# Optimization experiments

Hardware: AMD Instinct MI355X
Metric: run time of the kernel (lower is better)

## Reference

```python
import jax, jax.numpy as jnp
import numpy as np

EPS = 1e-06

def setup_inputs() -> dict:
    key = jax.random.key(0)
    k1, k2 = jax.random.split(key)
    x = jax.random.normal(k1, (8192, 4096), dtype=jnp.float32)
    # nn.Linear weight: [num_experts, input_dim]
    W = jax.random.normal(k2, (64, 4096), dtype=jnp.float32) * (1.0 / np.sqrt(4096.0))
    return {"x": x, "W": W}


def reference(x, W):
    # logits: [N, E]  (thin GEMM)
    logits = jnp.einsum('nd,ed->ne', x, W)
    gates = jax.nn.softmax(logits, axis=-1)
    # importance auxiliary loss: per-expert column sums, unbiased std (torch default)
    importance = gates.sum(axis=0)                      # [E]
    mean_imp = importance.mean()
    E = importance.shape[0]
    std_imp = jnp.sqrt(jnp.sum((importance - mean_imp) ** 2) / (E - 1))
    aux_loss = (std_imp / (mean_imp + EPS)) ** 2
    # top-k gates, renormalize with a second softmax
    top_k_gates, top_k_indices = jax.lax.top_k(gates, 2)  # [N, k]
    combine_weights = jax.nn.softmax(top_k_gates, axis=-1)
    return combine_weights, top_k_indices, aux_loss
```

## Files before the change

kernel.cpp:

```cpp
#include <hip/hip_runtime.h>
#include <math.h>

#define NROWS 8192
#define NK    4096
#define NE    64
#define NWV   8

typedef _Float16 f16x8 __attribute__((ext_vector_type(8)));
typedef float    f32x4 __attribute__((ext_vector_type(4)));

__global__ __launch_bounds__(256) void k_prep(const float* __restrict__ W,
                                              _Float16* __restrict__ Whi,
                                              _Float16* __restrict__ Wlo,
                                              float* __restrict__ imp) {
  const int idx = blockIdx.x * 256 + threadIdx.x;
  if (idx < NE) imp[idx] = 0.f;
  const int j    = idx & 7;
  const int lane = (idx >> 3) & 63;
  const int nt   = (idx >> 9) & 3;
  const int ksg  = idx >> 11;
  const int e = nt * 16 + (lane & 15);
  const int k = ksg * 32 + (lane >> 4) * 8 + j;
  const float w = W[(size_t)e * NK + k];
  const _Float16 wh = (_Float16)w;
  const _Float16 wl = (_Float16)(w - (float)wh);
  Whi[idx] = wh;
  Wlo[idx] = wl;
}

__global__ __launch_bounds__(512, 1) void k_fused(const float* __restrict__ x,
                                                  const _Float16* __restrict__ Whi,
                                                  const _Float16* __restrict__ Wlo,
                                                  float* __restrict__ out,
                                                  float* __restrict__ imp) {
  __shared__ float plds[NWV][32][64];
  __shared__ float logit[32][64];
  __shared__ float simp[NWV][64];

  const int tid  = threadIdx.x;
  const int lane = tid & 63;
  const int wv   = __builtin_amdgcn_readfirstlane(tid >> 6);
  const int l15  = lane & 15;
  const int lhi  = lane >> 4;
  const int rbase = blockIdx.x * 32;
  const int k0    = wv * 512;

  const float* __restrict__ xp0 = x + (size_t)(rbase + l15) * NK + k0 + lhi * 8;
  const float* __restrict__ xp1 = xp0 + (size_t)16 * NK;

  f32x4 acc0[4], acc1[4];
#pragma unroll
  for (int nt = 0; nt < 4; ++nt) {
    acc0[nt] = (f32x4){0.f, 0.f, 0.f, 0.f};
    acc1[nt] = (f32x4){0.f, 0.f, 0.f, 0.f};
  }

#pragma unroll 2
  for (int ks = 0; ks < 16; ++ks) {
    const float4 a0 = *(const float4*)(xp0 + ks * 32);
    const float4 a1 = *(const float4*)(xp0 + ks * 32 + 4);
    const float4 b0 = *(const float4*)(xp1 + ks * 32);
    const float4 b1 = *(const float4*)(xp1 + ks * 32 + 4);
    f16x8 ah, al, bh, bl;
    ah[0] = (_Float16)a0.x; al[0] = (_Float16)(a0.x - (float)ah[0]);
    ah[1] = (_Float16)a0.y; al[1] = (_Float16)(a0.y - (float)ah[1]);
    ah[2] = (_Float16)a0.z; al[2] = (_Float16)(a0.z - (float)ah[2]);
    ah[3] = (_Float16)a0.w; al[3] = (_Float16)(a0.w - (float)ah[3]);
    ah[4] = (_Float16)a1.x; al[4] = (_Float16)(a1.x - (float)ah[4]);
    ah[5] = (_Float16)a1.y; al[5] = (_Float16)(a1.y - (float)ah[5]);
    ah[6] = (_Float16)a1.z; al[6] = (_Float16)(a1.z - (float)ah[6]);
    ah[7] = (_Float16)a1.w; al[7] = (_Float16)(a1.w - (float)ah[7]);
    bh[0] = (_Float16)b0.x; bl[0] = (_Float16)(b0.x - (float)bh[0]);
    bh[1] = (_Float16)b0.y; bl[1] = (_Float16)(b0.y - (float)bh[1]);
    bh[2] = (_Float16)b0.z; bl[2] = (_Float16)(b0.z - (float)bh[2]);
    bh[3] = (_Float16)b0.w; bl[3] = (_Float16)(b0.w - (float)bh[3]);
    bh[4] = (_Float16)b1.x; bl[4] = (_Float16)(b1.x - (float)bh[4]);
    bh[5] = (_Float16)b1.y; bl[5] = (_Float16)(b1.y - (float)bh[5]);
    bh[6] = (_Float16)b1.z; bl[6] = (_Float16)(b1.z - (float)bh[6]);
    bh[7] = (_Float16)b1.w; bl[7] = (_Float16)(b1.w - (float)bh[7]);

    const int gk = wv * 16 + ks;
    const size_t boff = ((size_t)(gk * 4) * 64 + lane) * 8;
    f16x8 wh_[4], wl_[4];
#pragma unroll
    for (int nt = 0; nt < 4; ++nt) {
      wh_[nt] = *(const f16x8*)(Whi + boff + nt * 512);
      wl_[nt] = *(const f16x8*)(Wlo + boff + nt * 512);
    }
#pragma unroll
    for (int nt = 0; nt < 4; ++nt) {
      acc0[nt] = __builtin_amdgcn_mfma_f32_16x16x32_f16(ah, wh_[nt], acc0[nt], 0, 0, 0);
      acc1[nt] = __builtin_amdgcn_mfma_f32_16x16x32_f16(bh, wh_[nt], acc1[nt], 0, 0, 0);
    }
#pragma unroll
    for (int nt = 0; nt < 4; ++nt) {
      acc0[nt] = __builtin_amdgcn_mfma_f32_16x16x32_f16(ah, wl_[nt], acc0[nt], 0, 0, 0);
      acc1[nt] = __builtin_amdgcn_mfma_f32_16x16x32_f16(bh, wl_[nt], acc1[nt], 0, 0, 0);
    }
#pragma unroll
    for (int nt = 0; nt < 4; ++nt) {
      acc0[nt] = __builtin_amdgcn_mfma_f32_16x16x32_f16(al, wh_[nt], acc0[nt], 0, 0, 0);
      acc1[nt] = __builtin_amdgcn_mfma_f32_16x16x32_f16(bl, wh_[nt], acc1[nt], 0, 0, 0);
    }
  }

#pragma unroll
  for (int nt = 0; nt < 4; ++nt)
#pragma unroll
    for (int r = 0; r < 4; ++r) {
      plds[wv][lhi * 4 + r][nt * 16 + l15]      = acc0[nt][r];
      plds[wv][16 + lhi * 4 + r][nt * 16 + l15] = acc1[nt][r];
    }
  __syncthreads();

#pragma unroll
  for (int i = 0; i < 4; ++i) {
    const int elem = tid + i * 512;
    const int row  = elem >> 6;
    const int col  = elem & 63;
    const float s01 = plds[0][row][col] + plds[1][row][col];
    const float s23 = plds[2][row][col] + plds[3][row][col];
    const float s45 = plds[4][row][col] + plds[5][row][col];
    const float s67 = plds[6][row][col] + plds[7][row][col];
    logit[row][col] = ((s01 + s23) + (s45 + s67));
  }
  __syncthreads();

  float impacc = 0.f;
#pragma unroll 1
  for (int i = 0; i < 4; ++i) {
    const int rl  = wv * 4 + i;
    const int row = rbase + rl;
    const float lg = logit[rl][lane];

    float m = lg;
#pragma unroll
    for (int d = 1; d < 64; d <<= 1) m = fmaxf(m, __shfl_xor(m, d));
    float p = expf(lg - m);
    float s = p;
#pragma unroll
    for (int d = 1; d < 64; d <<= 1) s += __shfl_xor(s, d);
    const float gate = p / s;
    impacc += gate;

    const unsigned long long key =
        ((unsigned long long)__float_as_uint(gate) << 32) | (unsigned)(63 - lane);
    unsigned long long k1 = key;
#pragma unroll
    for (int d = 1; d < 64; d <<= 1) {
      unsigned long long o = __shfl_xor(k1, d);
      if (o > k1) k1 = o;
    }
    const int e1 = 63 - (int)(k1 & 63ull);
    unsigned long long k2 = (lane == e1) ? 0ull : key;
#pragma unroll
    for (int d = 1; d < 64; d <<= 1) {
      unsigned long long o = __shfl_xor(k2, d);
      if (o > k2) k2 = o;
    }
    const int e2 = 63 - (int)(k2 & 63ull);

    if (lane == 0) {
      const float g1 = __uint_as_float((unsigned)(k1 >> 32));
      const float g2 = __uint_as_float((unsigned)(k2 >> 32));
      const float tt  = expf(g2 - g1);
      const float inv = 1.f / (1.f + tt);
      out[(size_t)row * 2]     = inv;
      out[(size_t)row * 2 + 1] = tt * inv;
      out[(size_t)NROWS * 2 + row * 2]     = (float)e1;
      out[(size_t)NROWS * 2 + row * 2 + 1] = (float)e2;
    }
  }
  simp[wv][lane] = impacc;
  __syncthreads();

  if (tid < NE) {
    const float v = (((simp[0][tid] + simp[1][tid]) + (simp[2][tid] + simp[3][tid])) +
                     ((simp[4][tid] + simp[5][tid]) + (simp[6][tid] + simp[7][tid])));
    atomicAdd(&imp[tid], v);
  }
}

__global__ void k_aux(const float* __restrict__ imp, float* __restrict__ out) {
  const int lane = threadIdx.x;
  const float v = imp[lane];
  float s = v;
#pragma unroll
  for (int d = 1; d < 64; d <<= 1) s += __shfl_xor(s, d);
  const float mean = s / 64.f;
  const float dv = v - mean;
  float sq = dv * dv;
#pragma unroll
  for (int d = 1; d < 64; d <<= 1) sq += __shfl_xor(sq, d);
  const float stdv = sqrtf(sq / 63.f);
  const float r = stdv / (mean + 1e-6f);
  if (lane == 0) out[(size_t)NROWS * 4] = r * r;
}

extern "C" void kernel_launch(void* const* d_in, const int* in_sizes, int n_in,
                              void* d_out, int out_size, void* d_ws, size_t ws_size,
                              hipStream_t stream) {
  const float* x = (const float*)d_in[0];
  const float* W = (const float*)d_in[1];
  float* out  = (float*)d_out;
  _Float16* Whi = (_Float16*)d_ws;
  _Float16* Wlo = Whi + (size_t)NE * NK;
  float* imp  = (float*)(Wlo + (size_t)NE * NK);

  hipLaunchKernelGGL(k_prep,  dim3(1024), dim3(256), 0, stream, W, Whi, Wlo, imp);
  hipLaunchKernelGGL(k_fused, dim3(256),  dim3(512), 0, stream, x, Whi, Wlo, out, imp);
  hipLaunchKernelGGL(k_aux,   dim3(1),    dim3(64),  0, stream, imp, out);
}
```

Baseline: 49.34 us.

## Double waves per block for K-split and fold aux loss into fused kernel

Each block now runs 16 waves, each covering half as much of K, to raise memory-level parallelism when streaming x. The separate aux-loss kernel is removed: a global counter picks the last finishing block, which reads the importance sums atomically and computes the loss. This costs twice the LDS for partial sums, more cross-wave reduction work, and an extra atomic plus synchronisation at the end of every block.

```diff
diff --git a/kernel.cpp b/kernel.cpp
--- a/kernel.cpp
+++ b/kernel.cpp
@@ -4,7 +4,7 @@
 #define NROWS 8192
 #define NK    4096
 #define NE    64
-#define NWV   8
+#define NWV   16
 
 typedef _Float16 f16x8 __attribute__((ext_vector_type(8)));
 typedef float    f32x4 __attribute__((ext_vector_type(4)));
@@ -12,9 +12,11 @@
 __global__ __launch_bounds__(256) void k_prep(const float* __restrict__ W,
                                               _Float16* __restrict__ Whi,
                                               _Float16* __restrict__ Wlo,
-                                              float* __restrict__ imp) {
+                                              float* __restrict__ imp,
+                                              unsigned* __restrict__ cnt) {
   const int idx = blockIdx.x * 256 + threadIdx.x;
   if (idx < NE) imp[idx] = 0.f;
+  if (idx == NE) *cnt = 0u;
   const int j    = idx & 7;
   const int lane = (idx >> 3) & 63;
   const int nt   = (idx >> 9) & 3;
@@ -28,14 +30,16 @@
   Wlo[idx] = wl;
 }
 
-__global__ __launch_bounds__(512, 1) void k_fused(const float* __restrict__ x,
-                                                  const _Float16* __restrict__ Whi,
-                                                  const _Float16* __restrict__ Wlo,
-                                                  float* __restrict__ out,
-                                                  float* __restrict__ imp) {
+__global__ __launch_bounds__(1024, 4) void k_fused(const float* __restrict__ x,
+                                                   const _Float16* __restrict__ Whi,
+                                                   const _Float16* __restrict__ Wlo,
+                                                   float* __restrict__ out,
+                                                   float* __restrict__ imp,
+                                                   unsigned* __restrict__ cnt) {
   __shared__ float plds[NWV][32][64];
   __shared__ float logit[32][64];
   __shared__ float simp[NWV][64];
+  __shared__ int   lastflag;
 
   const int tid  = threadIdx.x;
   const int lane = tid & 63;
@@ -43,7 +47,7 @@
   const int l15  = lane & 15;
   const int lhi  = lane >> 4;
   const int rbase = blockIdx.x * 32;
-  const int k0    = wv * 512;
+  const int k0    = wv * 256;
 
   const float* __restrict__ xp0 = x + (size_t)(rbase + l15) * NK + k0 + lhi * 8;
   const float* __restrict__ xp1 = xp0 + (size_t)16 * NK;
@@ -55,8 +59,8 @@
     acc1[nt] = (f32x4){0.f, 0.f, 0.f, 0.f};
   }
 
-#pragma unroll 2
-  for (int ks = 0; ks < 16; ++ks) {
+#pragma unroll 1
+  for (int ks = 0; ks < 8; ++ks) {
     const float4 a0 = *(const float4*)(xp0 + ks * 32);
     const float4 a1 = *(const float4*)(xp0 + ks * 32 + 4);
     const float4 b0 = *(const float4*)(xp1 + ks * 32);
@@ -79,7 +83,7 @@
     bh[6] = (_Float16)b1.z; bl[6] = (_Float16)(b1.z - (float)bh[6]);
     bh[7] = (_Float16)b1.w; bl[7] = (_Float16)(b1.w - (float)bh[7]);
 
-    const int gk = wv * 16 + ks;
+    const int gk = wv * 8 + ks;
     const size_t boff = ((size_t)(gk * 4) * 64 + lane) * 8;
     f16x8 wh_[4], wl_[4];
 #pragma unroll
@@ -114,22 +118,23 @@
   __syncthreads();
 
 #pragma unroll
-  for (int i = 0; i < 4; ++i) {
-    const int elem = tid + i * 512;
+  for (int i = 0; i < 2; ++i) {
+    const int elem = tid + i * 1024;
     const int row  = elem >> 6;
     const int col  = elem & 63;
-    const float s01 = plds[0][row][col] + plds[1][row][col];
-    const float s23 = plds[2][row][col] + plds[3][row][col];
-    const float s45 = plds[4][row][col] + plds[5][row][col];
-    const float s67 = plds[6][row][col] + plds[7][row][col];
-    logit[row][col] = ((s01 + s23) + (s45 + s67));
+    float s[8];
+#pragma unroll
+    for (int p = 0; p < 8; ++p)
+      s[p] = plds[2 * p][row][col] + plds[2 * p + 1][row][col];
+    logit[row][col] = (((s[0] + s[1]) + (s[2] + s[3])) +
+                       ((s[4] + s[5]) + (s[6] + s[7])));
   }
   __syncthreads();
 
   float impacc = 0.f;
 #pragma unroll 1
-  for (int i = 0; i < 4; ++i) {
-    const int rl  = wv * 4 + i;
+  for (int i = 0; i < 2; ++i) {
+    const int rl  = wv * 2 + i;
     const int row = rbase + rl;
     const float lg = logit[rl][lane];
 
@@ -175,26 +180,33 @@
   __syncthreads();
 
   if (tid < NE) {
-    const float v = (((simp[0][tid] + simp[1][tid]) + (simp[2][tid] + simp[3][tid])) +
-                     ((simp[4][tid] + simp[5][tid]) + (simp[6][tid] + simp[7][tid])));
+    float v = 0.f;
+#pragma unroll
+    for (int p = 0; p < 8; ++p) v += simp[2 * p][tid] + simp[2 * p + 1][tid];
     atomicAdd(&imp[tid], v);
   }
-}
-
-__global__ void k_aux(const float* __restrict__ imp, float* __restrict__ out) {
-  const int lane = threadIdx.x;
-  const float v = imp[lane];
-  float s = v;
-#pragma unroll
-  for (int d = 1; d < 64; d <<= 1) s += __shfl_xor(s, d);
-  const float mean = s / 64.f;
-  const float dv = v - mean;
-  float sq = dv * dv;
-#pragma unroll
-  for (int d = 1; d < 64; d <<= 1) sq += __shfl_xor(sq, d);
-  const float stdv = sqrtf(sq / 63.f);
-  const float r = stdv / (mean + 1e-6f);
-  if (lane == 0) out[(size_t)NROWS * 4] = r * r;
+  __syncthreads();
+
+  if (tid == 0) {
+    const unsigned old = atomicAdd(cnt, 1u);
+    lastflag = (old == 255u) ? 1 : 0;
+  }
+  __syncthreads();
+
+  if (lastflag && tid < NE) {
+    const float v = atomicAdd(&imp[tid], 0.f);
+    float s = v;
+#pragma unroll
+    for (int d = 1; d < 64; d <<= 1) s += __shfl_xor(s, d);
+    const float mean = s / 64.f;
+    const float dv = v - mean;
+    float sq = dv * dv;
+#pragma unroll
+    for (int d = 1; d < 64; d <<= 1) sq += __shfl_xor(sq, d);
+    const float stdv = sqrtf(sq / 63.f);
+    const float r = stdv / (mean + 1e-6f);
+    if (tid == 0) out[(size_t)NROWS * 4] = r * r;
+  }
 }
 
 extern "C" void kernel_launch(void* const* d_in, const int* in_sizes, int n_in,
@@ -206,8 +218,8 @@
   _Float16* Whi = (_Float16*)d_ws;
   _Float16* Wlo = Whi + (size_t)NE * NK;
   float* imp  = (float*)(Wlo + (size_t)NE * NK);
-
-  hipLaunchKernelGGL(k_prep,  dim3(1024), dim3(256), 0, stream, W, Whi, Wlo, imp);
-  hipLaunchKernelGGL(k_fused, dim3(256),  dim3(512), 0, stream, x, Whi, Wlo, out, imp);
-  hipLaunchKernelGGL(k_aux,   dim3(1),    dim3(64),  0, stream, imp, out);
+  unsigned* cnt = (unsigned*)(imp + NE);
+
+  hipLaunchKernelGGL(k_prep,  dim3(1024), dim3(256),  0, stream, W, Whi, Wlo, imp, cnt);
+  hipLaunchKernelGGL(k_fused, dim3(256),  dim3(1024), 0, stream, x, Whi, Wlo, out, imp, cnt);
 }
```

After: 49.94 us. No clear change (+1.2%).

## Fuse weight prep, gating GEMM and aux loss into one kernel with flag sync

Applied to the files above, without the earlier changes.

Replaces the three-kernel sequence (weight split, fused GEMM+softmax+top-k, aux loss) with a single launch. The first 64 blocks split W into fp16 hi/lo halves and publish agent-scope release flags; all blocks spin on those flags before the GEMM. Each block writes its per-expert importance partials to a buffer, and the last block waits on per-block flags to reduce them and compute the aux loss. It also software-pipelines the x loads two k-steps ahead and fully unrolls the k loop. The aim is to remove inter-kernel launch gaps and the atomics, at the cost of spin-waits that assume all blocks are co-resident. The flags are never reset, so on repeated calls the waits pass immediately and may read stale weights or partials.

```diff
diff --git a/kernel.cpp b/kernel.cpp
--- a/kernel.cpp
+++ b/kernel.cpp
@@ -4,49 +4,82 @@
 #define NROWS 8192
 #define NK    4096
 #define NE    64
-#define NWV   8
+#define MAGIC 0x5A5A5A5Au
 
 typedef _Float16 f16x8 __attribute__((ext_vector_type(8)));
 typedef float    f32x4 __attribute__((ext_vector_type(4)));
 
-__global__ __launch_bounds__(256) void k_prep(const float* __restrict__ W,
-                                              _Float16* __restrict__ Whi,
-                                              _Float16* __restrict__ Wlo,
-                                              float* __restrict__ imp) {
-  const int idx = blockIdx.x * 256 + threadIdx.x;
-  if (idx < NE) imp[idx] = 0.f;
-  const int j    = idx & 7;
-  const int lane = (idx >> 3) & 63;
-  const int nt   = (idx >> 9) & 3;
-  const int ksg  = idx >> 11;
-  const int e = nt * 16 + (lane & 15);
-  const int k = ksg * 32 + (lane >> 4) * 8 + j;
-  const float w = W[(size_t)e * NK + k];
-  const _Float16 wh = (_Float16)w;
-  const _Float16 wl = (_Float16)(w - (float)wh);
-  Whi[idx] = wh;
-  Wlo[idx] = wl;
-}
-
-__global__ __launch_bounds__(512, 1) void k_fused(const float* __restrict__ x,
-                                                  const _Float16* __restrict__ Whi,
-                                                  const _Float16* __restrict__ Wlo,
-                                                  float* __restrict__ out,
-                                                  float* __restrict__ imp) {
-  __shared__ float plds[NWV][32][64];
+#define CVT8(H, L, V0, V1)                                            \
+  do {                                                                \
+    H[0] = (_Float16)V0.x; L[0] = (_Float16)(V0.x - (float)H[0]);     \
+    H[1] = (_Float16)V0.y; L[1] = (_Float16)(V0.y - (float)H[1]);     \
+    H[2] = (_Float16)V0.z; L[2] = (_Float16)(V0.z - (float)H[2]);     \
+    H[3] = (_Float16)V0.w; L[3] = (_Float16)(V0.w - (float)H[3]);     \
+    H[4] = (_Float16)V1.x; L[4] = (_Float16)(V1.x - (float)H[4]);     \
+    H[5] = (_Float16)V1.y; L[5] = (_Float16)(V1.y - (float)H[5]);     \
+    H[6] = (_Float16)V1.z; L[6] = (_Float16)(V1.z - (float)H[6]);     \
+    H[7] = (_Float16)V1.w; L[7] = (_Float16)(V1.w - (float)H[7]);     \
+  } while (0)
+
+__global__ __launch_bounds__(512, 2) void k_all(const float* __restrict__ x,
+                                                const float* __restrict__ W,
+                                                _Float16* __restrict__ Whi,
+                                                _Float16* __restrict__ Wlo,
+                                                unsigned* __restrict__ wflag,
+                                                float* __restrict__ impp,
+                                                unsigned* __restrict__ pflag,
+                                                float* __restrict__ out) {
+  __shared__ float plds[8][32][64];
   __shared__ float logit[32][64];
-  __shared__ float simp[NWV][64];
+  __shared__ float simp[8][64];
 
   const int tid  = threadIdx.x;
   const int lane = tid & 63;
   const int wv   = __builtin_amdgcn_readfirstlane(tid >> 6);
+  const int blk  = blockIdx.x;
   const int l15  = lane & 15;
   const int lhi  = lane >> 4;
-  const int rbase = blockIdx.x * 32;
+  const int rbase = blk * 32;
   const int k0    = wv * 512;
 
   const float* __restrict__ xp0 = x + (size_t)(rbase + l15) * NK + k0 + lhi * 8;
   const float* __restrict__ xp1 = xp0 + (size_t)16 * NK;
+
+  float4 ca0 = *(const float4*)(xp0);
+  float4 ca1 = *(const float4*)(xp0 + 4);
+  float4 cb0 = *(const float4*)(xp1);
+  float4 cb1 = *(const float4*)(xp1 + 4);
+  float4 na0 = *(const float4*)(xp0 + 32);
+  float4 na1 = *(const float4*)(xp0 + 36);
+  float4 nb0 = *(const float4*)(xp1 + 32);
+  float4 nb1 = *(const float4*)(xp1 + 36);
+
+  if (blk < 64) {
+    const int g    = blk * 512 + tid;
+    const int gl   = g & 63;
+    const int gnt  = (g >> 6) & 3;
+    const int gksg = g >> 8;
+    const int e  = gnt * 16 + (gl & 15);
+    const int kk = gksg * 32 + (gl >> 4) * 8;
+    const float* wsrc = W + (size_t)e * NK + kk;
+    const float4 w0 = *(const float4*)(wsrc);
+    const float4 w1 = *(const float4*)(wsrc + 4);
+    f16x8 hi, lo;
+    CVT8(hi, lo, w0, w1);
+    *(f16x8*)(Whi + (size_t)g * 8) = hi;
+    *(f16x8*)(Wlo + (size_t)g * 8) = lo;
+    __syncthreads();
+    if (tid == 0)
+      __hip_atomic_store(&wflag[blk], MAGIC, __ATOMIC_RELEASE,
+                         __HIP_MEMORY_SCOPE_AGENT);
+  }
+
+  if (wv == 0) {
+    while (__hip_atomic_load(&wflag[lane], __ATOMIC_ACQUIRE,
+                             __HIP_MEMORY_SCOPE_AGENT) != MAGIC)
+      __builtin_amdgcn_s_sleep(2);
+  }
+  __syncthreads();
 
   f32x4 acc0[4], acc1[4];
 #pragma unroll
@@ -55,29 +88,18 @@
     acc1[nt] = (f32x4){0.f, 0.f, 0.f, 0.f};
   }
 
-#pragma unroll 2
+#pragma unroll
   for (int ks = 0; ks < 16; ++ks) {
-    const float4 a0 = *(const float4*)(xp0 + ks * 32);
-    const float4 a1 = *(const float4*)(xp0 + ks * 32 + 4);
-    const float4 b0 = *(const float4*)(xp1 + ks * 32);
-    const float4 b1 = *(const float4*)(xp1 + ks * 32 + 4);
     f16x8 ah, al, bh, bl;
-    ah[0] = (_Float16)a0.x; al[0] = (_Float16)(a0.x - (float)ah[0]);
-    ah[1] = (_Float16)a0.y; al[1] = (_Float16)(a0.y - (float)ah[1]);
-    ah[2] = (_Float16)a0.z; al[2] = (_Float16)(a0.z - (float)ah[2]);
-    ah[3] = (_Float16)a0.w; al[3] = (_Float16)(a0.w - (float)ah[3]);
-    ah[4] = (_Float16)a1.x; al[4] = (_Float16)(a1.x - (float)ah[4]);
-    ah[5] = (_Float16)a1.y; al[5] = (_Float16)(a1.y - (float)ah[5]);
-    ah[6] = (_Float16)a1.z; al[6] = (_Float16)(a1.z - (float)ah[6]);
-    ah[7] = (_Float16)a1.w; al[7] = (_Float16)(a1.w - (float)ah[7]);
-    bh[0] = (_Float16)b0.x; bl[0] = (_Float16)(b0.x - (float)bh[0]);
-    bh[1] = (_Float16)b0.y; bl[1] = (_Float16)(b0.y - (float)bh[1]);
-    bh[2] = (_Float16)b0.z; bl[2] = (_Float16)(b0.z - (float)bh[2]);
-    bh[3] = (_Float16)b0.w; bl[3] = (_Float16)(b0.w - (float)bh[3]);
-    bh[4] = (_Float16)b1.x; bl[4] = (_Float16)(b1.x - (float)bh[4]);
-    bh[5] = (_Float16)b1.y; bl[5] = (_Float16)(b1.y - (float)bh[5]);
-    bh[6] = (_Float16)b1.z; bl[6] = (_Float16)(b1.z - (float)bh[6]);
-    bh[7] = (_Float16)b1.w; bl[7] = (_Float16)(b1.w - (float)bh[7]);
+    CVT8(ah, al, ca0, ca1);
+    CVT8(bh, bl, cb0, cb1);
+    ca0 = na0; ca1 = na1; cb0 = nb0; cb1 = nb1;
+    if (ks + 2 < 16) {
+      na0 = *(const float4*)(xp0 + (ks + 2) * 32);
+      na1 = *(const float4*)(xp0 + (ks + 2) * 32 + 4);
+      nb0 = *(const float4*)(xp1 + (ks + 2) * 32);
+      nb1 = *(const float4*)(xp1 + (ks + 2) * 32 + 4);
+    }
 
     const int gk = wv * 16 + ks;
     const size_t boff = ((size_t)(gk * 4) * 64 + lane) * 8;
@@ -177,24 +199,43 @@
   if (tid < NE) {
     const float v = (((simp[0][tid] + simp[1][tid]) + (simp[2][tid] + simp[3][tid])) +
                      ((simp[4][tid] + simp[5][tid]) + (simp[6][tid] + simp[7][tid])));
-    atomicAdd(&imp[tid], v);
-  }
-}
-
-__global__ void k_aux(const float* __restrict__ imp, float* __restrict__ out) {
-  const int lane = threadIdx.x;
-  const float v = imp[lane];
-  float s = v;
-#pragma unroll
-  for (int d = 1; d < 64; d <<= 1) s += __shfl_xor(s, d);
-  const float mean = s / 64.f;
-  const float dv = v - mean;
-  float sq = dv * dv;
-#pragma unroll
-  for (int d = 1; d < 64; d <<= 1) sq += __shfl_xor(sq, d);
-  const float stdv = sqrtf(sq / 63.f);
-  const float r = stdv / (mean + 1e-6f);
-  if (lane == 0) out[(size_t)NROWS * 4] = r * r;
+    impp[(size_t)tid * 256 + blk] = v;
+  }
+  __syncthreads();
+  if (tid == 0)
+    __hip_atomic_store(&pflag[blk], MAGIC, __ATOMIC_RELEASE,
+                       __HIP_MEMORY_SCOPE_AGENT);
+
+  if (blk == 255) {
+    if (wv == 0) {
+#pragma unroll
+      for (int q = 0; q < 4; ++q)
+        while (__hip_atomic_load(&pflag[lane + q * 64], __ATOMIC_ACQUIRE,
+                                 __HIP_MEMORY_SCOPE_AGENT) != MAGIC)
+          __builtin_amdgcn_s_sleep(2);
+    }
+    __syncthreads();
+    if (tid < NE) {
+      const float* pp = impp + (size_t)tid * 256;
+      float a0 = 0.f, a1 = 0.f, a2 = 0.f, a3 = 0.f;
+#pragma unroll 4
+      for (int b = 0; b < 256; b += 4) {
+        a0 += pp[b]; a1 += pp[b + 1]; a2 += pp[b + 2]; a3 += pp[b + 3];
+      }
+      const float v = (a0 + a1) + (a2 + a3);
+      float s = v;
+#pragma unroll
+      for (int d = 1; d < 64; d <<= 1) s += __shfl_xor(s, d);
+      const float mean = s / 64.f;
+      const float dv = v - mean;
+      float sq = dv * dv;
+#pragma unroll
+      for (int d = 1; d < 64; d <<= 1) sq += __shfl_xor(sq, d);
+      const float stdv = sqrtf(sq / 63.f);
+      const float r = stdv / (mean + 1e-6f);
+      if (tid == 0) out[(size_t)NROWS * 4] = r * r;
+    }
+  }
 }
 
 extern "C" void kernel_launch(void* const* d_in, const int* in_sizes, int n_in,
@@ -202,12 +243,14 @@
                               hipStream_t stream) {
   const float* x = (const float*)d_in[0];
   const float* W = (const float*)d_in[1];
-  float* out  = (float*)d_out;
-  _Float16* Whi = (_Float16*)d_ws;
-  _Float16* Wlo = Whi + (size_t)NE * NK;
-  float* imp  = (float*)(Wlo + (size_t)NE * NK);
-
-  hipLaunchKernelGGL(k_prep,  dim3(1024), dim3(256), 0, stream, W, Whi, Wlo, imp);
-  hipLaunchKernelGGL(k_fused, dim3(256),  dim3(512), 0, stream, x, Whi, Wlo, out, imp);
-  hipLaunchKernelGGL(k_aux,   dim3(1),    dim3(64),  0, stream, imp, out);
+  float* out = (float*)d_out;
+  char* ws = (char*)d_ws;
+  _Float16* Whi   = (_Float16*)(ws);
+  _Float16* Wlo   = (_Float16*)(ws + 524288);
+  float*    impp  = (float*)  (ws + 1048576);
+  unsigned* wflag = (unsigned*)(ws + 1114112);
+  unsigned* pflag = (unsigned*)(ws + 1114624);
+
+  hipLaunchKernelGGL(k_all, dim3(256), dim3(512), 0, stream,
+                     x, W, Whi, Wlo, wflag, impp, pflag, out);
 }
```

Result: slower. 53.59 us (+8.6%).

## Software-pipeline x and W loads with register double-buffering in fused GEMM loop

Applied to the files above, without the earlier changes.

The K loop is fully unrolled and explicitly prefetches x two iterations ahead and the split-f16 W fragments one iteration ahead into registers, so global load latency overlaps with MFMA work. Launch bounds change to allow two waves per EU, which trades register budget for more resident waves per CU. The deeper register buffering raises VGPR pressure and could cause spills under the tighter occupancy target.

```diff
diff --git a/kernel.cpp b/kernel.cpp
--- a/kernel.cpp
+++ b/kernel.cpp
@@ -8,6 +8,18 @@
 
 typedef _Float16 f16x8 __attribute__((ext_vector_type(8)));
 typedef float    f32x4 __attribute__((ext_vector_type(4)));
+
+#define CVT8(H, L, V0, V1)                                            \
+  do {                                                                \
+    H[0] = (_Float16)V0.x; L[0] = (_Float16)(V0.x - (float)H[0]);     \
+    H[1] = (_Float16)V0.y; L[1] = (_Float16)(V0.y - (float)H[1]);     \
+    H[2] = (_Float16)V0.z; L[2] = (_Float16)(V0.z - (float)H[2]);     \
+    H[3] = (_Float16)V0.w; L[3] = (_Float16)(V0.w - (float)H[3]);     \
+    H[4] = (_Float16)V1.x; L[4] = (_Float16)(V1.x - (float)H[4]);     \
+    H[5] = (_Float16)V1.y; L[5] = (_Float16)(V1.y - (float)H[5]);     \
+    H[6] = (_Float16)V1.z; L[6] = (_Float16)(V1.z - (float)H[6]);     \
+    H[7] = (_Float16)V1.w; L[7] = (_Float16)(V1.w - (float)H[7]);     \
+  } while (0)
 
 __global__ __launch_bounds__(256) void k_prep(const float* __restrict__ W,
                                               _Float16* __restrict__ Whi,
@@ -28,11 +40,13 @@
   Wlo[idx] = wl;
 }
 
-__global__ __launch_bounds__(512, 1) void k_fused(const float* __restrict__ x,
-                                                  const _Float16* __restrict__ Whi,
-                                                  const _Float16* __restrict__ Wlo,
-                                                  float* __restrict__ out,
-                                                  float* __restrict__ imp) {
+__global__ __launch_bounds__(512)
+__attribute__((amdgpu_waves_per_eu(2, 2)))
+void k_fused(const float* __restrict__ x,
+             const _Float16* __restrict__ Whi,
+             const _Float16* __restrict__ Wlo,
+             float* __restrict__ out,
+             float* __restrict__ imp) {
   __shared__ float plds[NWV][32][64];
   __shared__ float logit[32][64];
   __shared__ float simp[NWV][64];
@@ -47,6 +61,8 @@
 
   const float* __restrict__ xp0 = x + (size_t)(rbase + l15) * NK + k0 + lhi * 8;
   const float* __restrict__ xp1 = xp0 + (size_t)16 * NK;
+  const _Float16* __restrict__ whp = Whi + ((size_t)(wv * 16 * 4) * 64 + lane) * 8;
+  const _Float16* __restrict__ wlp = Wlo + ((size_t)(wv * 16 * 4) * 64 + lane) * 8;
 
   f32x4 acc0[4], acc1[4];
 #pragma unroll
@@ -55,53 +71,63 @@
     acc1[nt] = (f32x4){0.f, 0.f, 0.f, 0.f};
   }
 
-#pragma unroll 2
+  float4 ca0 = *(const float4*)(xp0);
+  float4 ca1 = *(const float4*)(xp0 + 4);
+  float4 cb0 = *(const float4*)(xp1);
+  float4 cb1 = *(const float4*)(xp1 + 4);
+  float4 na0 = *(const float4*)(xp0 + 32);
+  float4 na1 = *(const float4*)(xp0 + 36);
+  float4 nb0 = *(const float4*)(xp1 + 32);
+  float4 nb1 = *(const float4*)(xp1 + 36);
+  f16x8 whc[4], wlc[4], whn[4], wln[4];
+#pragma unroll
+  for (int nt = 0; nt < 4; ++nt) {
+    whc[nt] = *(const f16x8*)(whp + nt * 512);
+    wlc[nt] = *(const f16x8*)(wlp + nt * 512);
+  }
+
+#pragma unroll
   for (int ks = 0; ks < 16; ++ks) {
-    const float4 a0 = *(const float4*)(xp0 + ks * 32);
-    const float4 a1 = *(const float4*)(xp0 + ks * 32 + 4);
-    const float4 b0 = *(const float4*)(xp1 + ks * 32);
-    const float4 b1 = *(const float4*)(xp1 + ks * 32 + 4);
+    if (ks < 15) {
+      const size_t nb_ = (size_t)(ks + 1) * 2048;
+#pragma unroll
+      for (int nt = 0; nt < 4; ++nt) {
+        whn[nt] = *(const f16x8*)(whp + nb_ + nt * 512);
+        wln[nt] = *(const f16x8*)(wlp + nb_ + nt * 512);
+      }
+    }
+    float4 pa0, pa1, pb0, pb1;
+    if (ks + 2 < 16) {
+      pa0 = *(const float4*)(xp0 + (ks + 2) * 32);
+      pa1 = *(const float4*)(xp0 + (ks + 2) * 32 + 4);
+      pb0 = *(const float4*)(xp1 + (ks + 2) * 32);
+      pb1 = *(const float4*)(xp1 + (ks + 2) * 32 + 4);
+    }
+
     f16x8 ah, al, bh, bl;
-    ah[0] = (_Float16)a0.x; al[0] = (_Float16)(a0.x - (float)ah[0]);
-    ah[1] = (_Float16)a0.y; al[1] = (_Float16)(a0.y - (float)ah[1]);
-    ah[2] = (_Float16)a0.z; al[2] = (_Float16)(a0.z - (float)ah[2]);
-    ah[3] = (_Float16)a0.w; al[3] = (_Float16)(a0.w - (float)ah[3]);
-    ah[4] = (_Float16)a1.x; al[4] = (_Float16)(a1.x - (float)ah[4]);
-    ah[5] = (_Float16)a1.y; al[5] = (_Float16)(a1.y - (float)ah[5]);
-    ah[6] = (_Float16)a1.z; al[6] = (_Float16)(a1.z - (float)ah[6]);
-    ah[7] = (_Float16)a1.w; al[7] = (_Float16)(a1.w - (float)ah[7]);
-    bh[0] = (_Float16)b0.x; bl[0] = (_Float16)(b0.x - (float)bh[0]);
-    bh[1] = (_Float16)b0.y; bl[1] = (_Float16)(b0.y - (float)bh[1]);
-    bh[2] = (_Float16)b0.z; bl[2] = (_Float16)(b0.z - (float)bh[2]);
-    bh[3] = (_Float16)b0.w; bl[3] = (_Float16)(b0.w - (float)bh[3]);
-    bh[4] = (_Float16)b1.x; bl[4] = (_Float16)(b1.x - (float)bh[4]);
-    bh[5] = (_Float16)b1.y; bl[5] = (_Float16)(b1.y - (float)bh[5]);
-    bh[6] = (_Float16)b1.z; bl[6] = (_Float16)(b1.z - (float)bh[6]);
-    bh[7] = (_Float16)b1.w; bl[7] = (_Float16)(b1.w - (float)bh[7]);
-
-    const int gk = wv * 16 + ks;
-    const size_t boff = ((size_t)(gk * 4) * 64 + lane) * 8;
-    f16x8 wh_[4], wl_[4];
+    CVT8(ah, al, ca0, ca1);
+    CVT8(bh, bl, cb0, cb1);
+
 #pragma unroll
     for (int nt = 0; nt < 4; ++nt) {
-      wh_[nt] = *(const f16x8*)(Whi + boff + nt * 512);
-      wl_[nt] = *(const f16x8*)(Wlo + boff + nt * 512);
+      acc0[nt] = __builtin_amdgcn_mfma_f32_16x16x32_f16(ah, whc[nt], acc0[nt], 0, 0, 0);
+      acc1[nt] = __builtin_amdgcn_mfma_f32_16x16x32_f16(bh, whc[nt], acc1[nt], 0, 0, 0);
     }
 #pragma unroll
     for (int nt = 0; nt < 4; ++nt) {
-      acc0[nt] = __builtin_amdgcn_mfma_f32_16x16x32_f16(ah, wh_[nt], acc0[nt], 0, 0, 0);
-      acc1[nt] = __builtin_amdgcn_mfma_f32_16x16x32_f16(bh, wh_[nt], acc1[nt], 0, 0, 0);
+      acc0[nt] = __builtin_amdgcn_mfma_f32_16x16x32_f16(ah, wlc[nt], acc0[nt], 0, 0, 0);
+      acc1[nt] = __builtin_amdgcn_mfma_f32_16x16x32_f16(bh, wlc[nt], acc1[nt], 0, 0, 0);
     }
 #pragma unroll
     for (int nt = 0; nt < 4; ++nt) {
-      acc0[nt] = __builtin_amdgcn_mfma_f32_16x16x32_f16(ah, wl_[nt], acc0[nt], 0, 0, 0);
-      acc1[nt] = __builtin_amdgcn_mfma_f32_16x16x32_f16(bh, wl_[nt], acc1[nt], 0, 0, 0);
-    }
-#pragma unroll
-    for (int nt = 0; nt < 4; ++nt) {
-      acc0[nt] = __builtin_amdgcn_mfma_f32_16x16x32_f16(al, wh_[nt], acc0[nt], 0, 0, 0);
-      acc1[nt] = __builtin_amdgcn_mfma_f32_16x16x32_f16(bl, wh_[nt], acc1[nt], 0, 0, 0);
-    }
+      acc0[nt] = __builtin_amdgcn_mfma_f32_16x16x32_f16(al, whc[nt], acc0[nt], 0, 0, 0);
+      acc1[nt] = __builtin_amdgcn_mfma_f32_16x16x32_f16(bl, whc[nt], acc1[nt], 0, 0, 0);
+    }
+
+    ca0 = na0; ca1 = na1; cb0 = nb0; cb1 = nb1;
+    na0 = pa0; na1 = pa1; nb0 = pb0; nb1 = pb1;
+#pragma unroll
+    for (int nt = 0; nt < 4; ++nt) { whc[nt] = whn[nt]; wlc[nt] = wln[nt]; }
   }
 
 #pragma unroll
```

Result: faster. 47.89 us (-2.9%).
